# Performance work log

Hardware: AMD Instinct MI355X
Metric: run time of the kernel (lower is better)

Reference implementation:

```python
import jax, jax.numpy as jnp
import numpy as np

B, N, E, H = 4, 2048, 768, 8
D = E // H
SCALING = D ** (-0.5)


def setup_inputs() -> dict:
    key = jax.random.key(0)
    k0, k1, k2, k3, k4 = jax.random.split(key, 5)
    x = jax.random.normal(k0, (B, N, E), dtype=jnp.float32)
    Wqkv = jax.random.normal(k1, (E, 3 * E), dtype=jnp.float32) * 0.02
    bqkv = jax.random.normal(k2, (3 * E,), dtype=jnp.float32) * 0.02
    Wproj = jax.random.normal(k3, (E, E), dtype=jnp.float32) * 0.02
    bproj = jax.random.normal(k4, (E,), dtype=jnp.float32) * 0.02
    return {"x": x, "Wqkv": Wqkv, "bqkv": bqkv, "Wproj": Wproj, "bproj": bproj}


def reference(x, Wqkv, bqkv, Wproj, bproj):
    b, n, e = x.shape
    h, d = H, E // H
    # QKV projection: [b, n, 3e]
    qkv = x @ Wqkv + bqkv
    # rearrange 'b n (h d qkv) -> qkv b h n d': qkv is the INNERMOST axis
    qkv = qkv.reshape(b, n, h, d, 3)
    q = jnp.transpose(qkv[..., 0], (0, 2, 1, 3))  # [b, h, n, d]
    k = jnp.transpose(qkv[..., 1], (0, 2, 1, 3))
    v = jnp.transpose(qkv[..., 2], (0, 2, 1, 3))
    # unscaled attention scores, softmax, then post-softmax scaling (as in source)
    energy = jnp.einsum('bhqd,bhkd->bhqk', q, k)  # [b, h, n, n]
    att = jax.nn.softmax(energy, axis=-1) * SCALING
    out = jnp.einsum('bhqk,bhkd->bhqd', att, v)   # [b, h, n, d]
    out = jnp.transpose(out, (0, 2, 1, 3)).reshape(b, n, e)
    return out @ Wproj + bproj
```

## Files before the change

kernel.cpp:

```cpp
#include <hip/hip_runtime.h>
#include <cstdint>

#define BB 4
#define SEQ 2048
#define EMB 768
#define NH 8
#define HD 96
#define E3 2304
#define MTOK 8192
#define NROWS 65536
#define SCALING 0.10206207261596575f
#define LOG2E 1.44269504f

typedef unsigned short u16;
typedef unsigned int u32;
typedef __bf16 bf16x8 __attribute__((ext_vector_type(8)));
typedef float f32x4 __attribute__((ext_vector_type(4)));
typedef float f32x16 __attribute__((ext_vector_type(16)));

__device__ __forceinline__ u16 f2bf(float f) {
    union { float f; uint32_t u; } c; c.f = f;
    uint32_t u = c.u;
    return (u16)((u + 0x7FFFu + ((u >> 16) & 1u)) >> 16);
}
__device__ __forceinline__ u16 f2bf_fast(float f) {
    union { float f; uint32_t u; } c; c.f = f;
    return (u16)((c.u + 0x8000u) >> 16);
}
__device__ __forceinline__ uint32_t pk2(float a, float b) {
    return (uint32_t)f2bf(a) | ((uint32_t)f2bf(b) << 16);
}
__device__ __forceinline__ uint32_t pk2_fast(float a, float b) {
    return (uint32_t)f2bf_fast(a) | ((uint32_t)f2bf_fast(b) << 16);
}
__device__ __forceinline__ float bf2f(u16 h) {
    union { uint32_t u; float f; } c; c.u = ((uint32_t)h) << 16; return c.f;
}
__device__ __forceinline__ float fexp2(float x) {
    return __builtin_amdgcn_exp2f(x);
}
__device__ __forceinline__ void async16(const u16* g, u16* l) {
    __builtin_amdgcn_global_load_lds(
        (const __attribute__((address_space(1))) void*)g,
        (__attribute__((address_space(3))) void*)l, 16, 0, 0);
}


__global__ void cvt_x_kernel(const float* __restrict__ src, u16* __restrict__ dst, int n8) {
    int i = blockIdx.x * blockDim.x + threadIdx.x;
    if (i >= n8) return;
    const float4* s4 = (const float4*)src;
    float4 a = s4[2 * i];
    float4 c = s4[2 * i + 1];
    uint4 o;
    o.x = pk2(a.x, a.y); o.y = pk2(a.z, a.w);
    o.z = pk2(c.x, c.y); o.w = pk2(c.z, c.w);
    ((uint4*)dst)[i] = o;
}

__global__ __launch_bounds__(256) void transpose_w_kernel(const float* __restrict__ src,
                                                          u16* __restrict__ dst,
                                                          int ncols, int mode) {
    __shared__ float T[64][65];
    int j0 = blockIdx.x * 64, k0 = blockIdx.y * 64;
    int tid = threadIdx.x;
#pragma unroll
    for (int it = 0; it < 16; ++it) {
        int lin = it * 256 + tid;
        int rr2 = lin >> 6, jj = lin & 63;
        int j = j0 + jj;
        int c;
        if (mode == 0) c = j;
        else if (mode == 1) { int s = j / 768, rr = j % 768; c = (rr / 96) * 288 + (rr % 96) * 3 + s; }
        else { c = (j / 96) * 288 + (j % 96) * 3 + 2; }
        T[rr2][jj] = src[(k0 + rr2) * ncols + c];
    }
    __syncthreads();
#pragma unroll
    for (int it = 0; it < 16; ++it) {
        int lin = it * 256 + tid;
        int jr = lin >> 6, kc = lin & 63;
        dst[(size_t)(j0 + jr) * 768 + k0 + kc] = f2bf(T[kc][jr]);
    }
}


__device__ __forceinline__ void gemm_tiles(const u16* __restrict__ A,
                                           const u16* __restrict__ Bt,
                                           int m0, int n0, int tid,
                                           u16* As, u16* Bs, f32x4 acc[4][4]) {
    const int lane = tid & 63;
    const int w = tid >> 6;
    const int l15 = lane & 15;
    const int quad = lane >> 4;
    const int wr = (w >> 1) * 64;
    const int wc = (w & 1) * 64;
    const int swz = l15 & 7;
    for (int kb = 0; kb < 768; kb += 64) {
#pragma unroll
        for (int it = 0; it < 4; ++it) {
            int base = (w * 4 + it) * 64;
            int lin = base + lane;
            int row = lin >> 3, cl = lin & 7;
            int cg = cl ^ (row & 7);
            async16(&A[(size_t)(m0 + row) * 768 + kb + cg * 8], &As[base * 8]);
            async16(&Bt[(size_t)(n0 + row) * 768 + kb + cg * 8], &Bs[base * 8]);
        }
        __syncthreads();
#pragma unroll
        for (int ks = 0; ks < 2; ++ks) {
            bf16x8 af[4], bfg[4];
#pragma unroll
            for (int fi = 0; fi < 4; ++fi)
                af[fi] = *(const bf16x8*)&As[(wr + fi * 16 + l15) * 64 + (((ks * 4 + quad) ^ swz) * 8)];
#pragma unroll
            for (int fj = 0; fj < 4; ++fj)
                bfg[fj] = *(const bf16x8*)&Bs[(wc + fj * 16 + l15) * 64 + (((ks * 4 + quad) ^ swz) * 8)];
#pragma unroll
            for (int fi = 0; fi < 4; ++fi)
#pragma unroll
                for (int fj = 0; fj < 4; ++fj)
                    acc[fi][fj] = __builtin_amdgcn_mfma_f32_16x16x32_bf16(af[fi], bfg[fj], acc[fi][fj], 0, 0, 0);
        }
        __syncthreads();
    }
}

__device__ __forceinline__ void gemm_tiles64(const u16* __restrict__ A,
                                             const u16* __restrict__ Bt,
                                             int m0, int n0, int tid,
                                             u16* As, u16* Bs, f32x4 acc[4][2]) {
    const int lane = tid & 63;
    const int w = tid >> 6;
    const int l15 = lane & 15;
    const int quad = lane >> 4;
    const int wr = (w >> 1) * 64;
    const int wc = (w & 1) * 32;
    const int swz = l15 & 7;
    for (int kb = 0; kb < 768; kb += 64) {
#pragma unroll
        for (int it = 0; it < 4; ++it) {
            int base = (w * 4 + it) * 64;
            int lin = base + lane;
            int row = lin >> 3, cl = lin & 7;
            int cg = cl ^ (row & 7);
            async16(&A[(size_t)(m0 + row) * 768 + kb + cg * 8], &As[base * 8]);
        }
#pragma unroll
        for (int it = 0; it < 2; ++it) {
            int base = (w * 2 + it) * 64;
            int lin = base + lane;
            int row = lin >> 3, cl = lin & 7;
            int cg = cl ^ (row & 7);
            async16(&Bt[(size_t)(n0 + row) * 768 + kb + cg * 8], &Bs[base * 8]);
        }
        __syncthreads();
#pragma unroll
        for (int ks = 0; ks < 2; ++ks) {
            bf16x8 af[4], bfg[2];
#pragma unroll
            for (int fi = 0; fi < 4; ++fi)
                af[fi] = *(const bf16x8*)&As[(wr + fi * 16 + l15) * 64 + (((ks * 4 + quad) ^ swz) * 8)];
#pragma unroll
            for (int fj = 0; fj < 2; ++fj)
                bfg[fj] = *(const bf16x8*)&Bs[(wc + fj * 16 + l15) * 64 + (((ks * 4 + quad) ^ swz) * 8)];
#pragma unroll
            for (int fi = 0; fi < 4; ++fi)
#pragma unroll
                for (int fj = 0; fj < 2; ++fj)
                    acc[fi][fj] = __builtin_amdgcn_mfma_f32_16x16x32_bf16(af[fi], bfg[fj], acc[fi][fj], 0, 0, 0);
        }
        __syncthreads();
    }
}

__global__ __launch_bounds__(256) void gemm_qk_kernel(const u16* __restrict__ A,
                                                      const u16* __restrict__ Bt,
                                                      const float* __restrict__ bqkv,
                                                      u16* __restrict__ qb,
                                                      u16* __restrict__ kg) {
    __shared__ __align__(16) u16 As[128 * 64];
    __shared__ __align__(16) u16 Bs[128 * 64];
    int tid = threadIdx.x;
    int n0 = blockIdx.x * 128, m0 = blockIdx.y * 128;
    f32x4 acc[4][4] = {};
    gemm_tiles(A, Bt, m0, n0, tid, As, Bs, acc);
    int lane = tid & 63, w = tid >> 6, l15 = lane & 15, quad = lane >> 4;
    int wr = (w >> 1) * 64, wc = (w & 1) * 64;
#pragma unroll
    for (int fj = 0; fj < 4; ++fj) {
        int j = n0 + wc + fj * 16 + l15;
        int s = j / 768, rr = j % 768;
        int hh = rr / 96, dd = rr % 96;
        float bv = bqkv[hh * 288 + dd * 3 + s];
#pragma unroll
        for (int fi = 0; fi < 4; ++fi) {
#pragma unroll
            for (int r = 0; r < 4; ++r) {
                int m = m0 + wr + fi * 16 + quad * 4 + r;
                int b = m >> 11, n = m & 2047;
                int bh = b * NH + hh;
                float v = acc[fi][fj][r] + bv;
                if (s == 0) {
                    qb[((size_t)bh * SEQ + n) * HD + dd] = f2bf(v * LOG2E);
                } else {
                    int cp = (dd >> 3) ^ (n & 7);
                    kg[((size_t)bh * SEQ + n) * 128 + cp * 8 + (dd & 7)] = f2bf(v);
                }
            }
        }
    }
}

__global__ __launch_bounds__(256) void gemm_v_kernel(const u16* __restrict__ A,
                                                     const u16* __restrict__ Bt,
                                                     const float* __restrict__ bqkv,
                                                     u16* __restrict__ vt) {
    __shared__ __align__(16) u16 As[128 * 64];
    __shared__ __align__(16) u16 Bs[64 * 64];
    int tid = threadIdx.x;
    int n0 = blockIdx.x * 64, m0 = blockIdx.y * 128;
    f32x4 acc[4][2] = {};
    gemm_tiles64(A, Bt, m0, n0, tid, As, Bs, acc);
    int lane = tid & 63, w = tid >> 6, l15 = lane & 15, quad = lane >> 4;
    int wr = (w >> 1) * 64, wc = (w & 1) * 32;
    float bvs[4][4]; int hhs[4][4], dds[4][4];
#pragma unroll
    for (int fi = 0; fi < 4; ++fi)
#pragma unroll
        for (int r = 0; r < 4; ++r) {
            int m = m0 + wr + fi * 16 + quad * 4 + r;
            int hh = m / 96, dd = m % 96;
            hhs[fi][r] = hh; dds[fi][r] = dd;
            bvs[fi][r] = bqkv[hh * 288 + dd * 3 + 2];
        }
#pragma unroll
    for (int fj = 0; fj < 2; ++fj) {
        int n = n0 + wc + fj * 16 + l15;
        int b = n >> 11, nn = n & 2047;
#pragma unroll
        for (int fi = 0; fi < 4; ++fi) {
#pragma unroll
            for (int r = 0; r < 4; ++r) {
                int dd = dds[fi][r];
                int kk = (nn & ~63) | ((((nn >> 3) ^ dd) & 7) << 3) | (nn & 7);
                vt[((size_t)(b * NH + hhs[fi][r]) * HD + dd) * SEQ + kk] =
                    f2bf(acc[fi][fj][r] + bvs[fi][r]);
            }
        }
    }
}

__global__ __launch_bounds__(256) void gemm_proj_kernel(const u16* __restrict__ A,
                                                        const u16* __restrict__ Bt,
                                                        const float* __restrict__ bias,
                                                        float* __restrict__ out) {
    __shared__ __align__(16) u16 As[128 * 64];
    __shared__ __align__(16) u16 Bs[64 * 64];
    int tid = threadIdx.x;
    int n0 = blockIdx.x * 64, m0 = blockIdx.y * 128;
    f32x4 acc[4][2] = {};
    gemm_tiles64(A, Bt, m0, n0, tid, As, Bs, acc);
    int lane = tid & 63, w = tid >> 6, l15 = lane & 15, quad = lane >> 4;
    int wr = (w >> 1) * 64, wc = (w & 1) * 32;
#pragma unroll
    for (int fj = 0; fj < 2; ++fj) {
        int j = n0 + wc + fj * 16 + l15;
        float bv = bias[j];
#pragma unroll
        for (int fi = 0; fi < 4; ++fi) {
#pragma unroll
            for (int r = 0; r < 4; ++r) {
                int m = m0 + wr + fi * 16 + quad * 4 + r;
                out[(size_t)m * 768 + j] = acc[fi][fj][r] + bv;
            }
        }
    }
}

__global__ __launch_bounds__(256, 2) void attn_kernel(const u16* __restrict__ Q,
                                                      const u16* __restrict__ Kg,
                                                      const u16* __restrict__ Vt,
                                                      u16* __restrict__ part,
                                                      float* __restrict__ lpart) {
    __shared__ __align__(16) u16 Ks[2][64 * 128];
    __shared__ __align__(16) u16 Vs[2][96 * 64];
    int tid = threadIdx.x;
    int lane = tid & 63, w = tid >> 6;
    int l31 = lane & 31, hf = lane >> 5;
    int swz = l31 & 7;
    int qt = blockIdx.x, bh = blockIdx.y, kh = blockIdx.z;
    const u16* qp = Q + (size_t)bh * SEQ * HD;
    const u16* kgp = Kg + (size_t)bh * SEQ * 128;
    const u16* vtp = Vt + (size_t)bh * HD * SEQ;
    int qbase = qt * 256 + w * 64;
    int kbase = kh * 1024;

    bf16x8 aq[2][6];
#pragma unroll
    for (int j = 0; j < 2; ++j)
#pragma unroll
        for (int dc = 0; dc < 6; ++dc)
            aq[j][dc] = *(const bf16x8*)&qp[(size_t)(qbase + j * 32 + l31) * HD + dc * 16 + hf * 8];

    f32x16 Ot[2][3] = {};
    float lp[2] = {0.f, 0.f};

    auto stage = [&](int kt, int buf) {
        int k0 = kbase + kt * 64;
#pragma unroll
        for (int it = 0; it < 4; ++it) {
            int cw = w * 4 + it;
            async16(kgp + (size_t)(k0 + cw * 4 + (lane >> 4)) * 128 + (lane & 15) * 8,
                    &Ks[buf][cw * 512]);
        }
#pragma unroll
        for (int it = 0; it < 3; ++it) {
            int vw = w * 3 + it;
            async16(vtp + (size_t)(vw * 8 + (lane >> 3)) * SEQ + k0 + (lane & 7) * 8,
                    &Vs[buf][vw * 512]);
        }
    };

    stage(0, 0);
    __syncthreads();

    for (int kt = 0; kt < 16; ++kt) {
        int cur = kt & 1;
        if (kt + 1 < 16) stage(kt + 1, cur ^ 1);

#pragma unroll
        for (int tau = 0; tau < 2; ++tau) {
            f32x16 Sv0 = {}, Sv1 = {};
#pragma unroll
            for (int dc = 0; dc < 6; ++dc) {
                bf16x8 ka = *(const bf16x8*)&Ks[cur][(tau * 32 + l31) * 128 + (((2 * dc + hf) ^ swz) * 8)];
                Sv0 = __builtin_amdgcn_mfma_f32_32x32x16_bf16(ka, aq[0][dc], Sv0, 0, 0, 0);
                Sv1 = __builtin_amdgcn_mfma_f32_32x32x16_bf16(ka, aq[1][dc], Sv1, 0, 0, 0);
            }
            u32 pk[2][4][2];
#pragma unroll
            for (int g = 0; g < 4; ++g)
#pragma unroll
                for (int u = 0; u < 2; ++u) {
                    float a0 = fexp2(Sv0[g * 4 + 2 * u]);
                    float a1 = fexp2(Sv0[g * 4 + 2 * u + 1]);
                    lp[0] += a0 + a1;
                    pk[0][g][u] = pk2_fast(a0, a1);
                    float b0 = fexp2(Sv1[g * 4 + 2 * u]);
                    float b1 = fexp2(Sv1[g * 4 + 2 * u + 1]);
                    lp[1] += b0 + b1;
                    pk[1][g][u] = pk2_fast(b0, b1);
                }
            u32 rv[2][2][2];
#pragma unroll
            for (int j = 0; j < 2; ++j)
#pragma unroll
                for (int kc = 0; kc < 2; ++kc)
#pragma unroll
                    for (int u = 0; u < 2; ++u) {
                        u32 send = hf ? pk[j][2 * kc][u] : pk[j][2 * kc + 1][u];
                        rv[j][kc][u] = (u32)__shfl_xor((int)send, 32);
                    }
#pragma unroll
            for (int kc = 0; kc < 2; ++kc) {
                union { u32 u[4]; bf16x8 v; } pf0, pf1;
                pf0.u[0] = hf ? rv[0][kc][0] : pk[0][2 * kc][0];
                pf0.u[1] = hf ? rv[0][kc][1] : pk[0][2 * kc][1];
                pf0.u[2] = hf ? pk[0][2 * kc + 1][0] : rv[0][kc][0];
                pf0.u[3] = hf ? pk[0][2 * kc + 1][1] : rv[0][kc][1];
                pf1.u[0] = hf ? rv[1][kc][0] : pk[1][2 * kc][0];
                pf1.u[1] = hf ? rv[1][kc][1] : pk[1][2 * kc][1];
                pf1.u[2] = hf ? pk[1][2 * kc + 1][0] : rv[1][kc][0];
                pf1.u[3] = hf ? pk[1][2 * kc + 1][1] : rv[1][kc][1];
#pragma unroll
                for (int t = 0; t < 3; ++t) {
                    bf16x8 va = *(const bf16x8*)&Vs[cur][(t * 32 + l31) * 64 + (((4 * tau + 2 * kc + hf) ^ swz) * 8)];
                    Ot[0][t] = __builtin_amdgcn_mfma_f32_32x32x16_bf16(va, pf0.v, Ot[0][t], 0, 0, 0);
                    Ot[1][t] = __builtin_amdgcn_mfma_f32_32x32x16_bf16(va, pf1.v, Ot[1][t], 0, 0, 0);
                }
            }
        }
        __syncthreads();
    }

    size_t pb = (size_t)kh * NROWS + (size_t)bh * SEQ;
#pragma unroll
    for (int j = 0; j < 2; ++j) {
        int q = qbase + j * 32 + l31;
        float lr = lp[j] + __shfl_xor(lp[j], 32);
        if (hf == 0) lpart[(size_t)kh * NROWS + (size_t)bh * SEQ + q] = lr;
        size_t rowb = (pb + q) * HD;
#pragma unroll
        for (int t = 0; t < 3; ++t) {
#pragma unroll
            for (int g = 0; g < 4; ++g) {
                int d0 = t * 32 + 8 * g + 4 * hf;
                uint2 val;
                val.x = pk2(Ot[j][t][g * 4 + 0], Ot[j][t][g * 4 + 1]);
                val.y = pk2(Ot[j][t][g * 4 + 2], Ot[j][t][g * 4 + 3]);
                *(uint2*)&part[rowb + d0] = val;
            }
        }
    }
}

__global__ __launch_bounds__(256) void combine_kernel(const u16* __restrict__ part,
                                                      const float* __restrict__ lpart,
                                                      u16* __restrict__ ao) {
    int idx = blockIdx.x * 256 + threadIdx.x;
    int row = idx / 12, ch = idx % 12;
    float l = lpart[row] + lpart[NROWS + row];
    float sc = SCALING / l;
    const uint4 p0 = *(const uint4*)&part[(size_t)row * HD + ch * 8];
    const uint4 p1 = *(const uint4*)&part[((size_t)NROWS + row) * HD + ch * 8];
    const u16* a = (const u16*)&p0;
    const u16* bq = (const u16*)&p1;
    uint4 o;
    u32* ou = (u32*)&o;
#pragma unroll
    for (int i = 0; i < 4; ++i) {
        float e0 = (bf2f(a[2 * i]) + bf2f(bq[2 * i])) * sc;
        float e1 = (bf2f(a[2 * i + 1]) + bf2f(bq[2 * i + 1])) * sc;
        ou[i] = pk2(e0, e1);
    }
    int bh = row >> 11, n = row & 2047;
    int b = bh >> 3, h = bh & 7;
    *(uint4*)&ao[((size_t)(b * SEQ + n)) * EMB + h * HD + ch * 8] = o;
}


extern "C" void kernel_launch(void* const* d_in, const int* in_sizes, int n_in,
                              void* d_out, int out_size, void* d_ws, size_t ws_size,
                              hipStream_t stream) {
    const float* x     = (const float*)d_in[0];
    const float* Wqkv  = (const float*)d_in[1];
    const float* bqkv  = (const float*)d_in[2];
    const float* Wproj = (const float*)d_in[3];
    const float* bproj = (const float*)d_in[4];
    float* out = (float*)d_out;

    char* p = (char*)d_ws;
    u16*   xb    = (u16*)p;  p += (size_t)MTOK * EMB * 2;
    u16*   wqkT  = (u16*)p;  p += (size_t)1536 * EMB * 2;
    u16*   wvr   = (u16*)p;  p += (size_t)EMB * EMB * 2;
    u16*   wpt   = (u16*)p;  p += (size_t)EMB * EMB * 2;
    u16*   qb    = (u16*)p;  p += (size_t)MTOK * EMB * 2;
    u16*   kg    = (u16*)p;  p += (size_t)BB * NH * SEQ * 128 * 2;
    u16*   vt    = (u16*)p;  p += (size_t)MTOK * EMB * 2;
    u16*   ao    = (u16*)p;  p += (size_t)MTOK * EMB * 2;
    u16*   partb = (u16*)p;  p += (size_t)2 * NROWS * HD * 2;
    float* lpart = (float*)p; p += (size_t)2 * NROWS * 4;

    cvt_x_kernel<<<MTOK * EMB / 8 / 256, 256, 0, stream>>>(x, xb, MTOK * EMB / 8);
    transpose_w_kernel<<<dim3(1536 / 64, EMB / 64), 256, 0, stream>>>(Wqkv, wqkT, E3, 1);
    transpose_w_kernel<<<dim3(EMB / 64, EMB / 64), 256, 0, stream>>>(Wqkv, wvr, E3, 2);
    transpose_w_kernel<<<dim3(EMB / 64, EMB / 64), 256, 0, stream>>>(Wproj, wpt, EMB, 0);
    gemm_qk_kernel<<<dim3(1536 / 128, MTOK / 128), 256, 0, stream>>>(xb, wqkT, bqkv, qb, kg);
    gemm_v_kernel<<<dim3(MTOK / 64, EMB / 128), 256, 0, stream>>>(wvr, xb, bqkv, vt);
    attn_kernel<<<dim3(SEQ / 256, BB * NH, 2), 256, 0, stream>>>(qb, kg, vt, partb, lpart);
    combine_kernel<<<NROWS * 12 / 256, 256, 0, stream>>>(partb, lpart, ao);
    gemm_proj_kernel<<<dim3(EMB / 64, MTOK / 128), 256, 0, stream>>>(ao, wpt, bproj, out);
}
```

Baseline: 251.1 us.

## Split attention keys four ways, single-buffer LDS, fuse prep kernels

The key-range split in the attention kernel goes from 2 to 4 (512 keys per block). The grid becomes a flat 1D launch of 1024 blocks, ordered so the key splits of one head sit next to each other. K/V staging drops double buffering for a single LDS buffer with a sync after each load, which halves LDS use and may raise occupancy, but it loses load/compute overlap. The x conversion and the three weight transposes are merged into one prep kernel to save launches. The workspace is reorganised so the partial-output buffer aliases the dead prep buffers, and combine now sums four partials, which adds extra partial traffic.

```diff
diff --git a/kernel.cpp b/kernel.cpp
--- a/kernel.cpp
+++ b/kernel.cpp
@@ -9,6 +9,7 @@
 #define E3 2304
 #define MTOK 8192
 #define NROWS 65536
+#define KSPLIT 4
 #define SCALING 0.10206207261596575f
 #define LOG2E 1.44269504f
 
@@ -46,24 +47,10 @@
 }
 
 
-__global__ void cvt_x_kernel(const float* __restrict__ src, u16* __restrict__ dst, int n8) {
-    int i = blockIdx.x * blockDim.x + threadIdx.x;
-    if (i >= n8) return;
-    const float4* s4 = (const float4*)src;
-    float4 a = s4[2 * i];
-    float4 c = s4[2 * i + 1];
-    uint4 o;
-    o.x = pk2(a.x, a.y); o.y = pk2(a.z, a.w);
-    o.z = pk2(c.x, c.y); o.w = pk2(c.z, c.w);
-    ((uint4*)dst)[i] = o;
-}
-
-__global__ __launch_bounds__(256) void transpose_w_kernel(const float* __restrict__ src,
-                                                          u16* __restrict__ dst,
-                                                          int ncols, int mode) {
-    __shared__ float T[64][65];
-    int j0 = blockIdx.x * 64, k0 = blockIdx.y * 64;
-    int tid = threadIdx.x;
+__device__ __forceinline__ void transpose_body(const float* __restrict__ src,
+                                               u16* __restrict__ dst,
+                                               int ncols, int mode, int j0, int k0,
+                                               int tid, float (*T)[65]) {
 #pragma unroll
     for (int it = 0; it < 16; ++it) {
         int lin = it * 256 + tid;
@@ -81,6 +68,36 @@
         int lin = it * 256 + tid;
         int jr = lin >> 6, kc = lin & 63;
         dst[(size_t)(j0 + jr) * 768 + k0 + kc] = f2bf(T[kc][jr]);
+    }
+}
+
+__global__ __launch_bounds__(256) void prep_kernel(const float* __restrict__ x,
+                                                   const float* __restrict__ Wqkv,
+                                                   const float* __restrict__ Wproj,
+                                                   u16* __restrict__ xb,
+                                                   u16* __restrict__ wqkT,
+                                                   u16* __restrict__ wvr,
+                                                   u16* __restrict__ wpt) {
+    __shared__ float T[64][65];
+    int bid = blockIdx.x, tid = threadIdx.x;
+    if (bid < 3072) {
+        int i = bid * 256 + tid;
+        const float4* s4 = (const float4*)x;
+        float4 a = s4[2 * i];
+        float4 c = s4[2 * i + 1];
+        uint4 o;
+        o.x = pk2(a.x, a.y); o.y = pk2(a.z, a.w);
+        o.z = pk2(c.x, c.y); o.w = pk2(c.z, c.w);
+        ((uint4*)xb)[i] = o;
+    } else if (bid < 3360) {
+        int t = bid - 3072;
+        transpose_body(Wqkv, wqkT, E3, 1, (t % 24) * 64, (t / 24) * 64, tid, T);
+    } else if (bid < 3504) {
+        int t = bid - 3360;
+        transpose_body(Wqkv, wvr, E3, 2, (t % 12) * 64, (t / 12) * 64, tid, T);
+    } else {
+        int t = bid - 3504;
+        transpose_body(Wproj, wpt, EMB, 0, (t % 12) * 64, (t / 12) * 64, tid, T);
     }
 }
 
@@ -283,18 +300,21 @@
                                                       const u16* __restrict__ Vt,
                                                       u16* __restrict__ part,
                                                       float* __restrict__ lpart) {
-    __shared__ __align__(16) u16 Ks[2][64 * 128];
-    __shared__ __align__(16) u16 Vs[2][96 * 64];
+    __shared__ __align__(16) u16 Ks[64 * 128];
+    __shared__ __align__(16) u16 Vs[96 * 64];
     int tid = threadIdx.x;
     int lane = tid & 63, w = tid >> 6;
     int l31 = lane & 31, hf = lane >> 5;
     int swz = l31 & 7;
-    int qt = blockIdx.x, bh = blockIdx.y, kh = blockIdx.z;
+    int bid = blockIdx.x;
+    int qt = bid >> 7;
+    int g = bid & 127;
+    int bh = g >> 2, kh = g & 3;
     const u16* qp = Q + (size_t)bh * SEQ * HD;
     const u16* kgp = Kg + (size_t)bh * SEQ * 128;
     const u16* vtp = Vt + (size_t)bh * HD * SEQ;
     int qbase = qt * 256 + w * 64;
-    int kbase = kh * 1024;
+    int kbase = kh * 512;
 
     bf16x8 aq[2][6];
 #pragma unroll
@@ -306,51 +326,44 @@
     f32x16 Ot[2][3] = {};
     float lp[2] = {0.f, 0.f};
 
-    auto stage = [&](int kt, int buf) {
+    for (int kt = 0; kt < 8; ++kt) {
         int k0 = kbase + kt * 64;
 #pragma unroll
         for (int it = 0; it < 4; ++it) {
             int cw = w * 4 + it;
             async16(kgp + (size_t)(k0 + cw * 4 + (lane >> 4)) * 128 + (lane & 15) * 8,
-                    &Ks[buf][cw * 512]);
+                    &Ks[cw * 512]);
         }
 #pragma unroll
         for (int it = 0; it < 3; ++it) {
             int vw = w * 3 + it;
             async16(vtp + (size_t)(vw * 8 + (lane >> 3)) * SEQ + k0 + (lane & 7) * 8,
-                    &Vs[buf][vw * 512]);
-        }
-    };
-
-    stage(0, 0);
-    __syncthreads();
-
-    for (int kt = 0; kt < 16; ++kt) {
-        int cur = kt & 1;
-        if (kt + 1 < 16) stage(kt + 1, cur ^ 1);
+                    &Vs[vw * 512]);
+        }
+        __syncthreads();
 
 #pragma unroll
         for (int tau = 0; tau < 2; ++tau) {
             f32x16 Sv0 = {}, Sv1 = {};
 #pragma unroll
             for (int dc = 0; dc < 6; ++dc) {
-                bf16x8 ka = *(const bf16x8*)&Ks[cur][(tau * 32 + l31) * 128 + (((2 * dc + hf) ^ swz) * 8)];
+                bf16x8 ka = *(const bf16x8*)&Ks[(tau * 32 + l31) * 128 + (((2 * dc + hf) ^ swz) * 8)];
                 Sv0 = __builtin_amdgcn_mfma_f32_32x32x16_bf16(ka, aq[0][dc], Sv0, 0, 0, 0);
                 Sv1 = __builtin_amdgcn_mfma_f32_32x32x16_bf16(ka, aq[1][dc], Sv1, 0, 0, 0);
             }
             u32 pk[2][4][2];
 #pragma unroll
-            for (int g = 0; g < 4; ++g)
+            for (int g2 = 0; g2 < 4; ++g2)
 #pragma unroll
                 for (int u = 0; u < 2; ++u) {
-                    float a0 = fexp2(Sv0[g * 4 + 2 * u]);
-                    float a1 = fexp2(Sv0[g * 4 + 2 * u + 1]);
+                    float a0 = fexp2(Sv0[g2 * 4 + 2 * u]);
+                    float a1 = fexp2(Sv0[g2 * 4 + 2 * u + 1]);
                     lp[0] += a0 + a1;
-                    pk[0][g][u] = pk2_fast(a0, a1);
-                    float b0 = fexp2(Sv1[g * 4 + 2 * u]);
-                    float b1 = fexp2(Sv1[g * 4 + 2 * u + 1]);
+                    pk[0][g2][u] = pk2_fast(a0, a1);
+                    float b0 = fexp2(Sv1[g2 * 4 + 2 * u]);
+                    float b1 = fexp2(Sv1[g2 * 4 + 2 * u + 1]);
                     lp[1] += b0 + b1;
-                    pk[1][g][u] = pk2_fast(b0, b1);
+                    pk[1][g2][u] = pk2_fast(b0, b1);
                 }
             u32 rv[2][2][2];
 #pragma unroll
@@ -375,7 +388,7 @@
                 pf1.u[3] = hf ? pk[1][2 * kc + 1][1] : rv[1][kc][1];
 #pragma unroll
                 for (int t = 0; t < 3; ++t) {
-                    bf16x8 va = *(const bf16x8*)&Vs[cur][(t * 32 + l31) * 64 + (((4 * tau + 2 * kc + hf) ^ swz) * 8)];
+                    bf16x8 va = *(const bf16x8*)&Vs[(t * 32 + l31) * 64 + (((4 * tau + 2 * kc + hf) ^ swz) * 8)];
                     Ot[0][t] = __builtin_amdgcn_mfma_f32_32x32x16_bf16(va, pf0.v, Ot[0][t], 0, 0, 0);
                     Ot[1][t] = __builtin_amdgcn_mfma_f32_32x32x16_bf16(va, pf1.v, Ot[1][t], 0, 0, 0);
                 }
@@ -389,16 +402,16 @@
     for (int j = 0; j < 2; ++j) {
         int q = qbase + j * 32 + l31;
         float lr = lp[j] + __shfl_xor(lp[j], 32);
-        if (hf == 0) lpart[(size_t)kh * NROWS + (size_t)bh * SEQ + q] = lr;
+        if (hf == 0) lpart[pb + q] = lr;
         size_t rowb = (pb + q) * HD;
 #pragma unroll
         for (int t = 0; t < 3; ++t) {
 #pragma unroll
-            for (int g = 0; g < 4; ++g) {
-                int d0 = t * 32 + 8 * g + 4 * hf;
+            for (int g2 = 0; g2 < 4; ++g2) {
+                int d0 = t * 32 + 8 * g2 + 4 * hf;
                 uint2 val;
-                val.x = pk2(Ot[j][t][g * 4 + 0], Ot[j][t][g * 4 + 1]);
-                val.y = pk2(Ot[j][t][g * 4 + 2], Ot[j][t][g * 4 + 3]);
+                val.x = pk2(Ot[j][t][g2 * 4 + 0], Ot[j][t][g2 * 4 + 1]);
+                val.y = pk2(Ot[j][t][g2 * 4 + 2], Ot[j][t][g2 * 4 + 3]);
                 *(uint2*)&part[rowb + d0] = val;
             }
         }
@@ -410,20 +423,23 @@
                                                       u16* __restrict__ ao) {
     int idx = blockIdx.x * 256 + threadIdx.x;
     int row = idx / 12, ch = idx % 12;
-    float l = lpart[row] + lpart[NROWS + row];
+    float l = 0.f;
+#pragma unroll
+    for (int k = 0; k < KSPLIT; ++k) l += lpart[(size_t)k * NROWS + row];
     float sc = SCALING / l;
-    const uint4 p0 = *(const uint4*)&part[(size_t)row * HD + ch * 8];
-    const uint4 p1 = *(const uint4*)&part[((size_t)NROWS + row) * HD + ch * 8];
-    const u16* a = (const u16*)&p0;
-    const u16* bq = (const u16*)&p1;
+    float acc[8] = {};
+#pragma unroll
+    for (int k = 0; k < KSPLIT; ++k) {
+        uint4 pv = *(const uint4*)&part[((size_t)k * NROWS + row) * HD + ch * 8];
+        const u16* a = (const u16*)&pv;
+#pragma unroll
+        for (int i = 0; i < 8; ++i) acc[i] += bf2f(a[i]);
+    }
     uint4 o;
     u32* ou = (u32*)&o;
 #pragma unroll
-    for (int i = 0; i < 4; ++i) {
-        float e0 = (bf2f(a[2 * i]) + bf2f(bq[2 * i])) * sc;
-        float e1 = (bf2f(a[2 * i + 1]) + bf2f(bq[2 * i + 1])) * sc;
-        ou[i] = pk2(e0, e1);
-    }
+    for (int i = 0; i < 4; ++i)
+        ou[i] = pk2(acc[2 * i] * sc, acc[2 * i + 1] * sc);
     int bh = row >> 11, n = row & 2047;
     int b = bh >> 3, h = bh & 7;
     *(uint4*)&ao[((size_t)(b * SEQ + n)) * EMB + h * HD + ch * 8] = o;
@@ -441,24 +457,22 @@
     float* out = (float*)d_out;
 
     char* p = (char*)d_ws;
-    u16*   xb    = (u16*)p;  p += (size_t)MTOK * EMB * 2;
-    u16*   wqkT  = (u16*)p;  p += (size_t)1536 * EMB * 2;
-    u16*   wvr   = (u16*)p;  p += (size_t)EMB * EMB * 2;
+    u16*   qb    = (u16*)p;  p += (size_t)NROWS * HD * 2;
+    u16*   kg    = (u16*)p;  p += (size_t)NROWS * 128 * 2;
+    u16*   vt    = (u16*)p;  p += (size_t)NROWS * HD * 2;
+    u16*   ao    = (u16*)p;  p += (size_t)MTOK * EMB * 2;
     u16*   wpt   = (u16*)p;  p += (size_t)EMB * EMB * 2;
-    u16*   qb    = (u16*)p;  p += (size_t)MTOK * EMB * 2;
-    u16*   kg    = (u16*)p;  p += (size_t)BB * NH * SEQ * 128 * 2;
-    u16*   vt    = (u16*)p;  p += (size_t)MTOK * EMB * 2;
-    u16*   ao    = (u16*)p;  p += (size_t)MTOK * EMB * 2;
-    u16*   partb = (u16*)p;  p += (size_t)2 * NROWS * HD * 2;
-    float* lpart = (float*)p; p += (size_t)2 * NROWS * 4;
-
-    cvt_x_kernel<<<MTOK * EMB / 8 / 256, 256, 0, stream>>>(x, xb, MTOK * EMB / 8);
-    transpose_w_kernel<<<dim3(1536 / 64, EMB / 64), 256, 0, stream>>>(Wqkv, wqkT, E3, 1);
-    transpose_w_kernel<<<dim3(EMB / 64, EMB / 64), 256, 0, stream>>>(Wqkv, wvr, E3, 2);
-    transpose_w_kernel<<<dim3(EMB / 64, EMB / 64), 256, 0, stream>>>(Wproj, wpt, EMB, 0);
+    float* lpart = (float*)p; p += (size_t)KSPLIT * NROWS * 4;
+    char*  U     = p;
+    u16*   xb    = (u16*)U;
+    u16*   wqkT  = (u16*)(U + (size_t)MTOK * EMB * 2);
+    u16*   wvr   = (u16*)(U + (size_t)MTOK * EMB * 2 + (size_t)1536 * EMB * 2);
+    u16*   partb = (u16*)U;
+
+    prep_kernel<<<3648, 256, 0, stream>>>(x, Wqkv, Wproj, xb, wqkT, wvr, wpt);
     gemm_qk_kernel<<<dim3(1536 / 128, MTOK / 128), 256, 0, stream>>>(xb, wqkT, bqkv, qb, kg);
     gemm_v_kernel<<<dim3(MTOK / 64, EMB / 128), 256, 0, stream>>>(wvr, xb, bqkv, vt);
-    attn_kernel<<<dim3(SEQ / 256, BB * NH, 2), 256, 0, stream>>>(qb, kg, vt, partb, lpart);
+    attn_kernel<<<8 * 32 * KSPLIT, 256, 0, stream>>>(qb, kg, vt, partb, lpart);
     combine_kernel<<<NROWS * 12 / 256, 256, 0, stream>>>(partb, lpart, ao);
     gemm_proj_kernel<<<dim3(EMB / 64, MTOK / 128), 256, 0, stream>>>(ao, wpt, bproj, out);
 }
```

Measured after the change: 244.8 us. -2.5%, faster.
